# Optimization experiments

Hardware: AMD Instinct MI355X
Metric: run time of the kernel (lower is better)

The kernel has to match this reference:

```python
import jax, jax.numpy as jnp
import numpy as np
from jax import lax

B, L = 4, 1024
D_MODEL, D_STATE, D_CONV = 512, 16, 4
D_INNER = 2 * D_MODEL          # expand=2
DT_RANK = D_MODEL // 16        # ceil(512/16)=32
K_EXPERTS = 2                  # num_experts_per_token; only first k experts are used
EPS = 1e-5


def setup_inputs() -> dict:
    key = jax.random.key(0)
    ks = jax.random.split(key, 14)
    def n(k, shape, scale=0.02):
        return jax.random.normal(k, shape, jnp.float32) * scale
    # Mamba S4D-real init for A: A_log = log(1..d_state) broadcast over channels
    A_log = jnp.log(jnp.broadcast_to(jnp.arange(1, D_STATE + 1, dtype=jnp.float32), (D_INNER, D_STATE)))
    return {
        "x": jax.random.normal(ks[0], (B, L, D_MODEL), jnp.float32),
        "in_proj_w": n(ks[1], (2 * D_INNER, D_MODEL)),
        "conv_w": n(ks[2], (D_INNER, 1, D_CONV), 0.1),
        "conv_b": n(ks[3], (D_INNER,), 0.1),
        "x_proj_w": n(ks[4], (DT_RANK + 2 * D_STATE, D_INNER)),
        "dt_proj_w": n(ks[5], (D_INNER, DT_RANK), 0.1),
        "dt_proj_b": n(ks[6], (D_INNER,), 0.1),
        "A_log": A_log,
        "D_skip": jnp.ones((D_INNER,), jnp.float32),
        "out_proj_w": n(ks[7], (D_MODEL, D_INNER)),
        "moe_w1": n(ks[8], (K_EXPERTS, 2 * D_MODEL, D_MODEL)),
        "moe_b1": n(ks[9], (K_EXPERTS, 2 * D_MODEL)),
        "moe_w2": n(ks[10], (K_EXPERTS, D_MODEL, 2 * D_MODEL)),
        "moe_b2": n(ks[11], (K_EXPERTS, D_MODEL)),
    }


def _layernorm(x):
    # fresh nn.LayerNorm each forward: weight=1, bias=0, eps=1e-5
    mu = jnp.mean(x, -1, keepdims=True)
    var = jnp.mean(jnp.square(x - mu), -1, keepdims=True)
    return (x - mu) / jnp.sqrt(var + EPS)


def _mamba(x, in_proj_w, conv_w, conv_b, x_proj_w, dt_proj_w, dt_proj_b, A_log, D_skip, out_proj_w):
    b = x.shape[0]
    xz = x @ in_proj_w.T                               # (b, L, 2*d_inner)
    xc, z = jnp.split(xz, 2, axis=-1)
    # causal depthwise conv1d (torch pads both sides with d_conv-1 then slices [:L])
    conv = lax.conv_general_dilated(
        xc.transpose(0, 2, 1), conv_w, (1,), [(D_CONV - 1, 0)],
        feature_group_count=D_INNER) + conv_b[None, :, None]
    xs = jax.nn.silu(conv).transpose(0, 2, 1)          # (b, L, d_inner)
    dbc = xs @ x_proj_w.T                              # (b, L, dt_rank + 2*d_state)
    dt = dbc[..., :DT_RANK]
    Bm = dbc[..., DT_RANK:DT_RANK + D_STATE]           # (b, L, d_state)
    Cm = dbc[..., DT_RANK + D_STATE:]                  # (b, L, d_state)
    delta = jax.nn.softplus(dt @ dt_proj_w.T + dt_proj_b)  # (b, L, d_inner)
    A = -jnp.exp(A_log)                                # (d_inner, d_state)
    dA = jnp.exp(jnp.einsum('bld,dn->bldn', delta, A))     # (b, L, d_inner, d_state)
    dBx = (delta * xs)[..., None] * Bm[:, :, None, :]       # (b, L, d_inner, d_state)

    def step(h, inp):
        dA_t, dBx_t, C_t = inp
        h = dA_t * h + dBx_t                           # (b, d_inner, d_state)
        y = jnp.einsum('bdn,bn->bd', h, C_t)
        return h, y

    h0 = jnp.zeros((b, D_INNER, D_STATE), x.dtype)
    _, ys = lax.scan(step, h0, (dA.transpose(1, 0, 2, 3), dBx.transpose(1, 0, 2, 3), Cm.transpose(1, 0, 2)))
    y = ys.transpose(1, 0, 2) + xs * D_skip            # (b, L, d_inner)
    y = y * jax.nn.silu(z)
    return y @ out_proj_w.T                            # (b, L, d_model)


def reference(x, in_proj_w, conv_w, conv_b, x_proj_w, dt_proj_w, dt_proj_b,
              A_log, D_skip, out_proj_w, moe_w1, moe_b1, moe_w2, moe_b2):
    skip = x
    h = _layernorm(x)
    h = _mamba(h, in_proj_w, conv_w, conv_b, x_proj_w, dt_proj_w, dt_proj_b, A_log, D_skip, out_proj_w) + h
    h = _layernorm(h)
    # static 'MoE': unweighted average of the first K_EXPERTS dense FFNs
    a = jax.nn.relu(jnp.einsum('bld,ekd->belk', h, moe_w1) + moe_b1[None, :, None, :])
    moe = jnp.einsum('belk,edk->beld', a, moe_w2) + moe_b2[None, :, None, :]
    return jnp.mean(moe, axis=1) + skip
```

## Files before the change

kernel.cpp:

```cpp
#include <hip/hip_runtime.h>
#include <hip/hip_bf16.h>

#define BB 4
#define LL 1024
#define DM 512
#define DI 1024
#define DS 16
#define DTR 32
#define MM (BB*LL)

#define ACT_NONE 0
#define ACT_RELU 1
#define ACT_SP   2

#define CHUNK 32
#define NCH (LL/CHUNK)
#define NSTATE 65536

typedef __attribute__((ext_vector_type(8))) __bf16 bf16x8;
typedef __attribute__((ext_vector_type(8))) unsigned short us8;
typedef __attribute__((ext_vector_type(4))) float f32x4;

__device__ __forceinline__ unsigned short f2bf(float f) {
  union { float f; unsigned int u; } a; a.f = f;
  unsigned int r = a.u + 0x7fffu + ((a.u >> 16) & 1u);
  return (unsigned short)(r >> 16);
}
__device__ __forceinline__ float b2f(unsigned short u) {
  union { unsigned int i; float f; } a; a.i = (unsigned int)u << 16; return a.f;
}

__device__ __forceinline__ bf16x8 ld_frag(const unsigned short* p) {
  us8 s = *(const us8*)p;
  return __builtin_bit_cast(bf16x8, s);
}

__device__ __forceinline__ void gload16(const void* g, void* l) {
  __builtin_amdgcn_global_load_lds(
      (const __attribute__((address_space(1))) void*)g,
      (__attribute__((address_space(3))) void*)l, 16, 0, 0);
}

__global__ __launch_bounds__(256) void prep_ln_kernel(
    const float* __restrict__ x,
    const float* __restrict__ in_proj_w, const float* __restrict__ x_proj_w,
    const float* __restrict__ out_proj_w,
    const float* __restrict__ moe_w1,    const float* __restrict__ moe_w2,
    const float* __restrict__ moe_b2,
    float* __restrict__ h1, unsigned short* __restrict__ h1b,
    unsigned short* __restrict__ inpb,  unsigned short* __restrict__ xpjb,
    unsigned short* __restrict__ outpb,
    unsigned short* __restrict__ w1b,   unsigned short* __restrict__ w2cb,
    float* __restrict__ b2avg)
{
  __shared__ float red[8];
  int bid = blockIdx.x;
  if (bid < MM) {
    int row = bid;
    const float* p = x + (size_t)row * DM;
    float2 v = ((const float2*)p)[threadIdx.x];
    float s  = v.x + v.y;
    float ss = v.x*v.x + v.y*v.y;
    for (int o = 32; o; o >>= 1) { s += __shfl_down(s, o); ss += __shfl_down(ss, o); }
    int wid = threadIdx.x >> 6, lane = threadIdx.x & 63;
    if (lane == 0) { red[wid] = s; red[4+wid] = ss; }
    __syncthreads();
    s  = red[0]+red[1]+red[2]+red[3];
    ss = red[4]+red[5]+red[6]+red[7];
    float mu = s * (1.f/DM);
    float var = ss * (1.f/DM) - mu*mu;
    float rstd = rsqrtf(var + 1e-5f);
    float2 o2; o2.x = (v.x-mu)*rstd; o2.y = (v.y-mu)*rstd;
    ((float2*)(h1 + (size_t)row*DM))[threadIdx.x] = o2;
    ushort2 u; u.x = f2bf(o2.x); u.y = f2bf(o2.y);
    ((ushort2*)(h1b + (size_t)row*DM))[threadIdx.x] = u;
    return;
  }
  int i = (bid - MM) * 256 + threadIdx.x;
  int i4 = i * 4;
  auto cvt4 = [&](const float* src, unsigned short* dst) {
    float4 v = ((const float4*)src)[i];
    ushort4 o; o.x = f2bf(v.x); o.y = f2bf(v.y); o.z = f2bf(v.z); o.w = f2bf(v.w);
    ((ushort4*)dst)[i] = o;
  };
  if (i4 < 2*DI*DM) cvt4(in_proj_w, inpb);
  if (i4 < 64*DI)   cvt4(x_proj_w, xpjb);
  if (i4 < DM*DI)   cvt4(out_proj_w, outpb);
  if (i4 < 2*(2*DM)*DM) cvt4(moe_w1, w1b);
  if (i4 < DM*2*DI) {
    #pragma unroll
    for (int j = 0; j < 4; ++j) {
      int idx = i4 + j;
      int nrow = idx >> 11;
      int t = idx & (2*DI - 1);
      int e = t >> 10;
      int k = t & (DI - 1);
      w2cb[idx] = f2bf(moe_w2[((size_t)e*DM + nrow)*DI + k]);
    }
  }
  if (i4 < DM) {
    #pragma unroll
    for (int j = 0; j < 4; ++j)
      b2avg[i4+j] = 0.5f * (moe_b2[i4+j] + moe_b2[DM + i4+j]);
  }
}

__global__ __launch_bounds__(256) void ln_kernel(const float* __restrict__ in,
                                                 float* __restrict__ outf,
                                                 unsigned short* __restrict__ outb) {
  int row = blockIdx.x;
  const float* p = in + (size_t)row * DM;
  float2 v = ((const float2*)p)[threadIdx.x];
  float s  = v.x + v.y;
  float ss = v.x*v.x + v.y*v.y;
  for (int o = 32; o; o >>= 1) { s += __shfl_down(s, o); ss += __shfl_down(ss, o); }
  __shared__ float red[8];
  int wid = threadIdx.x >> 6, lane = threadIdx.x & 63;
  if (lane == 0) { red[wid] = s; red[4+wid] = ss; }
  __syncthreads();
  s  = red[0]+red[1]+red[2]+red[3];
  ss = red[4]+red[5]+red[6]+red[7];
  float mu = s * (1.f/DM);
  float var = ss * (1.f/DM) - mu*mu;
  float rstd = rsqrtf(var + 1e-5f);
  float2 o2; o2.x = (v.x-mu)*rstd; o2.y = (v.y-mu)*rstd;
  if (outf) ((float2*)(outf + (size_t)row*DM))[threadIdx.x] = o2;
  if (outb) {
    ushort2 u; u.x = f2bf(o2.x); u.y = f2bf(o2.y);
    ((ushort2*)(outb + (size_t)row*DM))[threadIdx.x] = u;
  }
}

template<int BM, int BN, int BK, int WR, int WC, int FM, int FN, int ACT,
         bool OUTF, bool OUTB>
__global__ __launch_bounds__(256) void gemm_mfma(
    const unsigned short* __restrict__ A, int lda,
    const unsigned short* __restrict__ B, int ldb,
    const float* __restrict__ bias,
    const float* __restrict__ res, int ldres,
    float* __restrict__ Cf, unsigned short* __restrict__ Cb, int ldc,
    int K, float scale, int nbx)
{
  static_assert(WR*WC == 4 && WR*FM*16 == BM && WC*FN*16 == BN, "geom");
  constexpr int ATILE = BM*BK, BTILE = BN*BK;
  constexpr int AL = ATILE/2048, BL = BTILE/2048;
  constexpr bool SWZ = (BK == 64);
  __shared__ unsigned short As[2*ATILE];
  __shared__ unsigned short Bs[2*BTILE];
  const int tid = threadIdx.x;
  const int nwg = gridDim.x;
  const int bid = blockIdx.x;
  const int cpx = nwg >> 3;
  const int wid = ((nwg & 7) == 0) ? ((bid & 7)*cpx + (bid >> 3)) : bid;
  const int bm = (wid / nbx) * BM;
  const int bn = (wid % nbx) * BN;
  const int w = tid >> 6, lane = tid & 63;
  const int wr = w / WC, wc = w % WC;
  const int rl = lane & 15, kg = lane >> 4;

  auto stage = [&](int buf, int k0) {
    #pragma unroll
    for (int it = 0; it < AL; ++it) {
      int o = (it*256 + tid) * 16;
      int os = SWZ ? (o ^ (((o>>7)&7)<<4)) : o;
      int e = os >> 1;
      int r = e / BK, c = e % BK;
      gload16(A + (size_t)(bm + r)*lda + k0 + c, (char*)As + buf*ATILE*2 + o);
    }
    #pragma unroll
    for (int it = 0; it < BL; ++it) {
      int o = (it*256 + tid) * 16;
      int os = SWZ ? (o ^ (((o>>7)&7)<<4)) : o;
      int e = os >> 1;
      int r = e / BK, c = e % BK;
      gload16(B + (size_t)(bn + r)*ldb + k0 + c, (char*)Bs + buf*BTILE*2 + o);
    }
  };

  f32x4 acc[FM][FN];
  #pragma unroll
  for (int m = 0; m < FM; ++m)
    #pragma unroll
    for (int n = 0; n < FN; ++n) { f32x4 z = {0.f,0.f,0.f,0.f}; acc[m][n] = z; }

  auto compute = [&](int buf) {
    #pragma unroll
    for (int kk = 0; kk < BK/32; ++kk) {
      bf16x8 af[FM], bfv[FN];
      #pragma unroll
      for (int m = 0; m < FM; ++m) {
        int byte = ((wr*FM*16 + m*16 + rl)*BK + kk*32 + kg*8) * 2;
        if (SWZ) byte ^= ((byte>>7)&7)<<4;
        af[m] = ld_frag((const unsigned short*)((const char*)As + buf*ATILE*2 + byte));
      }
      #pragma unroll
      for (int n = 0; n < FN; ++n) {
        int byte = ((wc*FN*16 + n*16 + rl)*BK + kk*32 + kg*8) * 2;
        if (SWZ) byte ^= ((byte>>7)&7)<<4;
        bfv[n] = ld_frag((const unsigned short*)((const char*)Bs + buf*BTILE*2 + byte));
      }
      #pragma unroll
      for (int m = 0; m < FM; ++m)
        #pragma unroll
        for (int n = 0; n < FN; ++n)
          acc[m][n] = __builtin_amdgcn_mfma_f32_16x16x32_bf16(af[m], bfv[n], acc[m][n], 0, 0, 0);
    }
  };

  stage(0, 0);
  const int nk = K / BK;
  for (int it = 0; it < nk; ++it) {
    if (it + 1 < nk) {
      stage((it&1)^1, (it+1)*BK);
      asm volatile("s_waitcnt vmcnt(%0)" :: "i"(AL+BL) : "memory");
    } else {
      asm volatile("s_waitcnt vmcnt(0)" ::: "memory");
    }
    __builtin_amdgcn_s_barrier();
    compute(it & 1);
    __builtin_amdgcn_s_barrier();
  }

  #pragma unroll
  for (int m = 0; m < FM; ++m) {
    int row = bm + wr*FM*16 + m*16 + kg*4;
    #pragma unroll
    for (int n = 0; n < FN; ++n) {
      int col = bn + wc*FN*16 + n*16 + rl;
      float bv = bias ? bias[col] : 0.f;
      #pragma unroll
      for (int j = 0; j < 4; ++j) {
        float v = acc[m][n][j] * scale + bv;
        if (ACT == ACT_RELU) v = fmaxf(v, 0.f);
        if (ACT == ACT_SP)   v = fmaxf(v, 0.f) + log1pf(__expf(-fabsf(v)));
        if (res) v += res[(size_t)(row + j)*ldres + col];
        size_t off = (size_t)(row + j)*ldc + col;
        if (OUTF) Cf[off] = v;
        if (OUTB) Cb[off] = f2bf(v);
      }
    }
  }
}

__global__ __launch_bounds__(256) void conv_silu_kernel(
    const unsigned short* __restrict__ xzb, const float* __restrict__ conv_w,
    const float* __restrict__ conv_b, unsigned short* __restrict__ xsb)
{
  int t = blockIdx.x * 256 + threadIdx.x;
  int d8 = (t & (DI/8 - 1)) * 8;
  int l = (t >> 7) & (LL-1);
  int b = t >> 17;
  size_t base = (size_t)(b*LL) * 2*DI + d8;
  float acc[8];
  #pragma unroll
  for (int j = 0; j < 8; ++j) acc[j] = conv_b[d8+j];
  #pragma unroll
  for (int k = 0; k < 4; ++k) {
    int ll = l - 3 + k;
    if (ll >= 0) {
      us8 v = *(const us8*)(xzb + base + (size_t)ll * 2*DI);
      #pragma unroll
      for (int j = 0; j < 8; ++j)
        acc[j] = fmaf(conv_w[(d8+j)*4 + k], b2f((unsigned short)v[j]), acc[j]);
    }
  }
  us8 o;
  #pragma unroll
  for (int j = 0; j < 8; ++j) {
    float s = acc[j];
    float v = s / (1.f + __expf(-s));
    o[j] = (unsigned short)f2bf(v);
  }
  *(us8*)(xsb + (size_t)((b*LL + l)*DI) + d8) = o;
}

__global__ __launch_bounds__(256) void scan_A(
    const unsigned short* __restrict__ deltab,
    const unsigned short* __restrict__ xsb,
    const float* __restrict__ dbc,
    const float* __restrict__ A_log,
    float* __restrict__ S, float* __restrict__ Qb)
{
  int blk = blockIdx.x;
  int dq = blk & 3;
  int c  = (blk >> 2) & (NCH-1);
  int b  = blk >> 7;
  int tid = threadIdx.x;
  int d = dq*256 + tid;
  float An[16];
  #pragma unroll
  for (int n = 0; n < 16; n += 4) {
    float4 a = *(const float4*)(A_log + d*DS + n);
    An[n+0] = -__expf(a.x) * 1.44269504f;
    An[n+1] = -__expf(a.y) * 1.44269504f;
    An[n+2] = -__expf(a.z) * 1.44269504f;
    An[n+3] = -__expf(a.w) * 1.44269504f;
  }
  __shared__ float s_B[CHUNK][16];
  for (int i = tid; i < CHUNK*16; i += 256) {
    int l = i >> 4, n = i & 15;
    s_B[l][n] = dbc[((size_t)(b*LL) + c*CHUNK + l)*64 + 32 + n];
  }
  __syncthreads();
  float h[16];
  #pragma unroll
  for (int n = 0; n < 16; ++n) h[n] = 0.f;
  float Ssum = 0.f;
  size_t rowbase = ((size_t)(b*LL) + c*CHUNK)*DI + d;
  #pragma unroll 4
  for (int l = 0; l < CHUNK; ++l) {
    float delta = b2f(deltab[rowbase + (size_t)l*DI]);
    float xv    = b2f(xsb   [rowbase + (size_t)l*DI]);
    float dx = delta * xv;
    Ssum += delta;
    #pragma unroll
    for (int n = 0; n < 16; ++n)
      h[n] = fmaf(exp2f(delta*An[n]), h[n], dx * s_B[l][n]);
  }
  S[c*(BB*DI) + b*DI + d] = Ssum;
  float* q = Qb + (size_t)c*NSTATE + (size_t)(b*DI + d)*16;
  #pragma unroll
  for (int n = 0; n < 16; n += 4) {
    float4 v; v.x = h[n]; v.y = h[n+1]; v.z = h[n+2]; v.w = h[n+3];
    *(float4*)(q + n) = v;
  }
}

__global__ __launch_bounds__(256) void scan_stitch(
    const float* __restrict__ S, const float* __restrict__ Qb,
    const float* __restrict__ A_log, float* __restrict__ H)
{
  int t = blockIdx.x * 256 + threadIdx.x;
  int bd = t >> 4, n = t & 15;
  int d = bd & (DI-1);
  float An = -__expf(A_log[d*DS + n]) * 1.44269504f;
  float h = 0.f;
  for (int c = 0; c < NCH; ++c) {
    H[(size_t)c*NSTATE + t] = h;
    h = fmaf(exp2f(S[c*(BB*DI) + bd]*An), h, Qb[(size_t)c*NSTATE + t]);
  }
}

__global__ __launch_bounds__(256) void scan_B(
    const unsigned short* __restrict__ deltab,
    const unsigned short* __restrict__ xsb,
    const unsigned short* __restrict__ xzb,
    const float* __restrict__ dbc,
    const float* __restrict__ A_log,
    const float* __restrict__ D_skip,
    const float* __restrict__ H,
    unsigned short* __restrict__ ymulb)
{
  int blk = blockIdx.x;
  int dq = blk & 3;
  int c  = (blk >> 2) & (NCH-1);
  int b  = blk >> 7;
  int tid = threadIdx.x;
  int d = dq*256 + tid;
  float An[16];
  #pragma unroll
  for (int n = 0; n < 16; n += 4) {
    float4 a = *(const float4*)(A_log + d*DS + n);
    An[n+0] = -__expf(a.x) * 1.44269504f;
    An[n+1] = -__expf(a.y) * 1.44269504f;
    An[n+2] = -__expf(a.z) * 1.44269504f;
    An[n+3] = -__expf(a.w) * 1.44269504f;
  }
  float Dd = D_skip[d];
  __shared__ float s_B[CHUNK][16], s_C[CHUNK][16];
  for (int i = tid; i < CHUNK*16; i += 256) {
    int l = i >> 4, n = i & 15;
    size_t row = (size_t)(b*LL) + c*CHUNK + l;
    s_B[l][n] = dbc[row*64 + 32 + n];
    s_C[l][n] = dbc[row*64 + 48 + n];
  }
  __syncthreads();
  float h[16];
  const float* hp = H + (size_t)c*NSTATE + (size_t)(b*DI + d)*16;
  #pragma unroll
  for (int n = 0; n < 16; n += 4) {
    float4 v = *(const float4*)(hp + n);
    h[n] = v.x; h[n+1] = v.y; h[n+2] = v.z; h[n+3] = v.w;
  }
  size_t rowbase = ((size_t)(b*LL) + c*CHUNK)*DI + d;
  size_t zbase   = ((size_t)(b*LL) + c*CHUNK)*2*DI + DI + d;
  #pragma unroll 4
  for (int l = 0; l < CHUNK; ++l) {
    float delta = b2f(deltab[rowbase + (size_t)l*DI]);
    float xv    = b2f(xsb   [rowbase + (size_t)l*DI]);
    float zv    = b2f(xzb   [zbase   + (size_t)l*2*DI]);
    float dx = delta * xv;
    float y = 0.f;
    #pragma unroll
    for (int n = 0; n < 16; ++n) {
      h[n] = fmaf(exp2f(delta*An[n]), h[n], dx * s_B[l][n]);
      y = fmaf(h[n], s_C[l][n], y);
    }
    float sz = zv / (1.f + __expf(-zv));
    float v = (y + xv*Dd) * sz;
    ymulb[rowbase + (size_t)l*DI] = f2bf(v);
  }
}

extern "C" void kernel_launch(void* const* d_in, const int* in_sizes, int n_in,
                              void* d_out, int out_size, void* d_ws, size_t ws_size,
                              hipStream_t stream) {
  const float* x         = (const float*)d_in[0];
  const float* in_proj_w = (const float*)d_in[1];
  const float* conv_w    = (const float*)d_in[2];
  const float* conv_b    = (const float*)d_in[3];
  const float* x_proj_w  = (const float*)d_in[4];
  const float* dt_proj_w = (const float*)d_in[5];
  const float* dt_proj_b = (const float*)d_in[6];
  const float* A_log     = (const float*)d_in[7];
  const float* D_skip    = (const float*)d_in[8];
  const float* out_proj_w= (const float*)d_in[9];
  const float* moe_w1    = (const float*)d_in[10];
  const float* moe_b1    = (const float*)d_in[11];
  const float* moe_w2    = (const float*)d_in[12];
  const float* moe_b2    = (const float*)d_in[13];
  float* out = (float*)d_out;

  float* p = (float*)d_ws;
  float* h1    = p; p += 2097152;
  float* h2    = p; p += 2097152;
  float* dbc   = p; p += 262144;
  float* Sbuf  = p; p += 131072;
  float* Qbuf  = p; p += 2097152;
  float* Hbuf  = p; p += 2097152;
  float* b2avg = p; p += 1024;
  unsigned short* h1b    = (unsigned short*)p; p += 1048576;
  unsigned short* xzb    = (unsigned short*)p; p += 4194304;
  unsigned short* xsb    = (unsigned short*)p; p += 2097152;
  unsigned short* deltab = (unsigned short*)p; p += 2097152;
  unsigned short* dbcb   = (unsigned short*)p; p += 131072;
  unsigned short* ymulb  = (unsigned short*)p; p += 2097152;
  unsigned short* h2lnb  = (unsigned short*)p; p += 1048576;
  unsigned short* acatb  = (unsigned short*)p; p += 4194304;
  unsigned short* inpb   = (unsigned short*)p; p += 524288;
  unsigned short* xpjb   = (unsigned short*)p; p += 32768;
  unsigned short* dtpb   = (unsigned short*)p; p += 16384;
  unsigned short* outpb  = (unsigned short*)p; p += 262144;
  unsigned short* w1b    = (unsigned short*)p; p += 524288;
  unsigned short* w2cb   = (unsigned short*)p; p += 524288;

  prep_ln_kernel<<<MM + 1024, 256, 0, stream>>>(x, in_proj_w, x_proj_w, out_proj_w,
                                                moe_w1, moe_w2, moe_b2,
                                                h1, h1b, inpb, xpjb, outpb, w1b, w2cb, b2avg);
  {
    struct K { static __global__ void f(const float* s, unsigned short* d) {
      int i = blockIdx.x*256 + threadIdx.x;
      if (i < 32768/4) {
        float4 v = ((const float4*)s)[i];
        ushort4 o; o.x = f2bf(v.x); o.y = f2bf(v.y); o.z = f2bf(v.z); o.w = f2bf(v.w);
        ((ushort4*)d)[i] = o;
      }
    }};
    K::f<<<32, 256, 0, stream>>>(dt_proj_w, dtpb);
  }
  gemm_mfma<128,128,64,2,2,4,4,ACT_NONE,false,true><<<512, 256, 0, stream>>>(
      h1b, DM, inpb, DM, nullptr, nullptr, 0, nullptr, xzb, 2*DI, DM, 1.f, 16);
  conv_silu_kernel<<<(MM*DI/8)/256, 256, 0, stream>>>(xzb, conv_w, conv_b, xsb);
  gemm_mfma<64,64,64,2,2,2,2,ACT_NONE,true,true><<<64, 256, 0, stream>>>(
      xsb, DI, xpjb, DI, nullptr, nullptr, 0, dbc, dbcb, 64, DI, 1.f, 1);
  gemm_mfma<128,128,32,2,2,4,4,ACT_SP,false,true><<<256, 256, 0, stream>>>(
      dbcb, 64, dtpb, DTR, dt_proj_b, nullptr, 0, nullptr, deltab, DI, DTR, 1.f, 8);
  scan_A<<<BB*NCH*4, 256, 0, stream>>>(deltab, xsb, dbc, A_log, Sbuf, Qbuf);
  scan_stitch<<<NSTATE/256, 256, 0, stream>>>(Sbuf, Qbuf, A_log, Hbuf);
  scan_B<<<BB*NCH*4, 256, 0, stream>>>(deltab, xsb, xzb, dbc, A_log, D_skip, Hbuf, ymulb);
  gemm_mfma<64,64,64,2,2,2,2,ACT_NONE,true,false><<<512, 256, 0, stream>>>(
      ymulb, DI, outpb, DI, nullptr, h1, DM, h2, nullptr, DM, DI, 1.f, 8);
  ln_kernel<<<MM, 256, 0, stream>>>(h2, nullptr, h2lnb);
  gemm_mfma<128,128,64,2,2,4,4,ACT_RELU,false,true><<<512, 256, 0, stream>>>(
      h2lnb, DM, w1b, DM, moe_b1, nullptr, 0, nullptr, acatb, 2*DI, DM, 1.f, 16);
  gemm_mfma<64,64,64,2,2,2,2,ACT_NONE,true,false><<<512, 256, 0, stream>>>(
      acatb, 2*DI, w2cb, 2*DI, b2avg, x, DM, out, nullptr, DM, 2*DI, 0.5f, 8);
}
```

Measured before the change: 223.1 us.

## Vectorize GEMM epilogue, raise BK to 128 for small GEMMs, fold dt_proj conversion

Swaps the MFMA operand order so each lane holds four consecutive output columns of one row. The epilogue can then do float4 bias and residual loads and float4/ushort4 stores instead of scalar strided ones. It also raises BK to 128 for the three 64x64-tile GEMMs, with a matching swizzle shift, which halves the number of k-iterations and barriers at the cost of more LDS per block. The separate dt_proj_w conversion kernel is folded into the prep kernel to save one launch.

```diff
diff --git a/kernel.cpp b/kernel.cpp
--- a/kernel.cpp
+++ b/kernel.cpp
@@ -44,12 +44,12 @@
 __global__ __launch_bounds__(256) void prep_ln_kernel(
     const float* __restrict__ x,
     const float* __restrict__ in_proj_w, const float* __restrict__ x_proj_w,
-    const float* __restrict__ out_proj_w,
+    const float* __restrict__ dt_proj_w, const float* __restrict__ out_proj_w,
     const float* __restrict__ moe_w1,    const float* __restrict__ moe_w2,
     const float* __restrict__ moe_b2,
     float* __restrict__ h1, unsigned short* __restrict__ h1b,
     unsigned short* __restrict__ inpb,  unsigned short* __restrict__ xpjb,
-    unsigned short* __restrict__ outpb,
+    unsigned short* __restrict__ dtpb,  unsigned short* __restrict__ outpb,
     unsigned short* __restrict__ w1b,   unsigned short* __restrict__ w2cb,
     float* __restrict__ b2avg)
 {
@@ -85,6 +85,7 @@
   };
   if (i4 < 2*DI*DM) cvt4(in_proj_w, inpb);
   if (i4 < 64*DI)   cvt4(x_proj_w, xpjb);
+  if (i4 < DI*DTR)  cvt4(dt_proj_w, dtpb);
   if (i4 < DM*DI)   cvt4(out_proj_w, outpb);
   if (i4 < 2*(2*DM)*DM) cvt4(moe_w1, w1b);
   if (i4 < DM*2*DI) {
@@ -144,7 +145,8 @@
   static_assert(WR*WC == 4 && WR*FM*16 == BM && WC*FN*16 == BN, "geom");
   constexpr int ATILE = BM*BK, BTILE = BN*BK;
   constexpr int AL = ATILE/2048, BL = BTILE/2048;
-  constexpr bool SWZ = (BK == 64);
+  constexpr bool SWZ = (BK >= 64);
+  constexpr int SH = (BK == 64) ? 7 : 8;
   __shared__ unsigned short As[2*ATILE];
   __shared__ unsigned short Bs[2*BTILE];
   const int tid = threadIdx.x;
@@ -162,7 +164,7 @@
     #pragma unroll
     for (int it = 0; it < AL; ++it) {
       int o = (it*256 + tid) * 16;
-      int os = SWZ ? (o ^ (((o>>7)&7)<<4)) : o;
+      int os = SWZ ? (o ^ (((o>>SH)&7)<<4)) : o;
       int e = os >> 1;
       int r = e / BK, c = e % BK;
       gload16(A + (size_t)(bm + r)*lda + k0 + c, (char*)As + buf*ATILE*2 + o);
@@ -170,7 +172,7 @@
     #pragma unroll
     for (int it = 0; it < BL; ++it) {
       int o = (it*256 + tid) * 16;
-      int os = SWZ ? (o ^ (((o>>7)&7)<<4)) : o;
+      int os = SWZ ? (o ^ (((o>>SH)&7)<<4)) : o;
       int e = os >> 1;
       int r = e / BK, c = e % BK;
       gload16(B + (size_t)(bn + r)*ldb + k0 + c, (char*)Bs + buf*BTILE*2 + o);
@@ -190,20 +192,20 @@
       #pragma unroll
       for (int m = 0; m < FM; ++m) {
         int byte = ((wr*FM*16 + m*16 + rl)*BK + kk*32 + kg*8) * 2;
-        if (SWZ) byte ^= ((byte>>7)&7)<<4;
+        if (SWZ) byte ^= ((byte>>SH)&7)<<4;
         af[m] = ld_frag((const unsigned short*)((const char*)As + buf*ATILE*2 + byte));
       }
       #pragma unroll
       for (int n = 0; n < FN; ++n) {
         int byte = ((wc*FN*16 + n*16 + rl)*BK + kk*32 + kg*8) * 2;
-        if (SWZ) byte ^= ((byte>>7)&7)<<4;
+        if (SWZ) byte ^= ((byte>>SH)&7)<<4;
         bfv[n] = ld_frag((const unsigned short*)((const char*)Bs + buf*BTILE*2 + byte));
       }
       #pragma unroll
       for (int m = 0; m < FM; ++m)
         #pragma unroll
         for (int n = 0; n < FN; ++n)
-          acc[m][n] = __builtin_amdgcn_mfma_f32_16x16x32_bf16(af[m], bfv[n], acc[m][n], 0, 0, 0);
+          acc[m][n] = __builtin_amdgcn_mfma_f32_16x16x32_bf16(bfv[n], af[m], acc[m][n], 0, 0, 0);
     }
   };
 
@@ -223,20 +225,33 @@
 
   #pragma unroll
   for (int m = 0; m < FM; ++m) {
-    int row = bm + wr*FM*16 + m*16 + kg*4;
+    int row = bm + wr*FM*16 + m*16 + rl;
     #pragma unroll
     for (int n = 0; n < FN; ++n) {
-      int col = bn + wc*FN*16 + n*16 + rl;
-      float bv = bias ? bias[col] : 0.f;
+      int colb = bn + wc*FN*16 + n*16 + kg*4;
+      float4 bv = {0.f,0.f,0.f,0.f};
+      if (bias) bv = *(const float4*)(bias + colb);
+      float vv[4];
       #pragma unroll
       for (int j = 0; j < 4; ++j) {
-        float v = acc[m][n][j] * scale + bv;
+        float v = acc[m][n][j] * scale + (&bv.x)[j];
         if (ACT == ACT_RELU) v = fmaxf(v, 0.f);
         if (ACT == ACT_SP)   v = fmaxf(v, 0.f) + log1pf(__expf(-fabsf(v)));
-        if (res) v += res[(size_t)(row + j)*ldres + col];
-        size_t off = (size_t)(row + j)*ldc + col;
-        if (OUTF) Cf[off] = v;
-        if (OUTB) Cb[off] = f2bf(v);
+        vv[j] = v;
+      }
+      if (res) {
+        float4 r = *(const float4*)(res + (size_t)row*ldres + colb);
+        vv[0] += r.x; vv[1] += r.y; vv[2] += r.z; vv[3] += r.w;
+      }
+      size_t off = (size_t)row*ldc + colb;
+      if (OUTF) {
+        float4 o; o.x = vv[0]; o.y = vv[1]; o.z = vv[2]; o.w = vv[3];
+        *(float4*)(Cf + off) = o;
+      }
+      if (OUTB) {
+        ushort4 o; o.x = f2bf(vv[0]); o.y = f2bf(vv[1]);
+        o.z = f2bf(vv[2]); o.w = f2bf(vv[3]);
+        *(ushort4*)(Cb + off) = o;
       }
     }
   }
@@ -444,35 +459,25 @@
   unsigned short* w1b    = (unsigned short*)p; p += 524288;
   unsigned short* w2cb   = (unsigned short*)p; p += 524288;
 
-  prep_ln_kernel<<<MM + 1024, 256, 0, stream>>>(x, in_proj_w, x_proj_w, out_proj_w,
-                                                moe_w1, moe_w2, moe_b2,
-                                                h1, h1b, inpb, xpjb, outpb, w1b, w2cb, b2avg);
-  {
-    struct K { static __global__ void f(const float* s, unsigned short* d) {
-      int i = blockIdx.x*256 + threadIdx.x;
-      if (i < 32768/4) {
-        float4 v = ((const float4*)s)[i];
-        ushort4 o; o.x = f2bf(v.x); o.y = f2bf(v.y); o.z = f2bf(v.z); o.w = f2bf(v.w);
-        ((ushort4*)d)[i] = o;
-      }
-    }};
-    K::f<<<32, 256, 0, stream>>>(dt_proj_w, dtpb);
-  }
+  prep_ln_kernel<<<MM + 1024, 256, 0, stream>>>(x, in_proj_w, x_proj_w, dt_proj_w,
+                                                out_proj_w, moe_w1, moe_w2, moe_b2,
+                                                h1, h1b, inpb, xpjb, dtpb, outpb,
+                                                w1b, w2cb, b2avg);
   gemm_mfma<128,128,64,2,2,4,4,ACT_NONE,false,true><<<512, 256, 0, stream>>>(
       h1b, DM, inpb, DM, nullptr, nullptr, 0, nullptr, xzb, 2*DI, DM, 1.f, 16);
   conv_silu_kernel<<<(MM*DI/8)/256, 256, 0, stream>>>(xzb, conv_w, conv_b, xsb);
-  gemm_mfma<64,64,64,2,2,2,2,ACT_NONE,true,true><<<64, 256, 0, stream>>>(
+  gemm_mfma<64,64,128,2,2,2,2,ACT_NONE,true,true><<<64, 256, 0, stream>>>(
       xsb, DI, xpjb, DI, nullptr, nullptr, 0, dbc, dbcb, 64, DI, 1.f, 1);
   gemm_mfma<128,128,32,2,2,4,4,ACT_SP,false,true><<<256, 256, 0, stream>>>(
       dbcb, 64, dtpb, DTR, dt_proj_b, nullptr, 0, nullptr, deltab, DI, DTR, 1.f, 8);
   scan_A<<<BB*NCH*4, 256, 0, stream>>>(deltab, xsb, dbc, A_log, Sbuf, Qbuf);
   scan_stitch<<<NSTATE/256, 256, 0, stream>>>(Sbuf, Qbuf, A_log, Hbuf);
   scan_B<<<BB*NCH*4, 256, 0, stream>>>(deltab, xsb, xzb, dbc, A_log, D_skip, Hbuf, ymulb);
-  gemm_mfma<64,64,64,2,2,2,2,ACT_NONE,true,false><<<512, 256, 0, stream>>>(
+  gemm_mfma<64,64,128,2,2,2,2,ACT_NONE,true,false><<<512, 256, 0, stream>>>(
       ymulb, DI, outpb, DI, nullptr, h1, DM, h2, nullptr, DM, DI, 1.f, 8);
   ln_kernel<<<MM, 256, 0, stream>>>(h2, nullptr, h2lnb);
   gemm_mfma<128,128,64,2,2,4,4,ACT_RELU,false,true><<<512, 256, 0, stream>>>(
       h2lnb, DM, w1b, DM, moe_b1, nullptr, 0, nullptr, acatb, 2*DI, DM, 1.f, 16);
-  gemm_mfma<64,64,64,2,2,2,2,ACT_NONE,true,false><<<512, 256, 0, stream>>>(
+  gemm_mfma<64,64,128,2,2,2,2,ACT_NONE,true,false><<<512, 256, 0, stream>>>(
       acatb, 2*DI, w2cb, 2*DI, b2avg, x, DM, out, nullptr, DM, 2*DI, 0.5f, 8);
 }
```

Result: faster. 210.8 us (-5.5%).
